# Kernel optimization log

Hardware: AMD Instinct MI355X
Metric: run time of the kernel (lower is better)

Reference implementation:

```python
import jax, jax.numpy as jnp
import numpy as np

NUM_LEVELS = 8
BASE_RES = 16
MAX_RES = 1024
TABLE_SIZE = 2 ** 17
FEAT = 2
ALPHA_SHIFT = 5.0
ALPHA_SCALE = 1.0

_growth = np.exp((np.log(MAX_RES) - np.log(BASE_RES)) / (NUM_LEVELS - 1))
SCALINGS = np.floor(BASE_RES * _growth ** np.arange(NUM_LEVELS)).astype(np.float32)  # per-level grid res
CORNERS = np.array([[(i >> 2) & 1, (i >> 1) & 1, i & 1] for i in range(8)], dtype=np.int32)  # voxel corners
PRIMES = np.array([1, 2654435761, 805459861], dtype=np.uint32)  # nerfstudio hash primes


def hash_encode(pos, table):
    # pos: [N,3] in [0,1]; table: [NUM_LEVELS*TABLE_SIZE, FEAT]
    scaled = pos[:, None, :] * jnp.asarray(SCALINGS)[None, :, None]              # [N,L,3]
    f = jnp.floor(scaled)
    w = scaled - f                                                               # trilinear weights
    idx = f.astype(jnp.int32)[:, :, None, :] + jnp.asarray(CORNERS)[None, None]  # [N,L,8,3]
    h = idx.astype(jnp.uint32) * jnp.asarray(PRIMES)
    hashed = (h[..., 0] ^ h[..., 1] ^ h[..., 2]) % TABLE_SIZE                    # [N,L,8]
    hashed = hashed.astype(jnp.int32) + (jnp.arange(NUM_LEVELS, dtype=jnp.int32) * TABLE_SIZE)[None, :, None]
    feats = table[hashed]                                                        # [N,L,8,F] gather
    cw = jnp.where(jnp.asarray(CORNERS)[None, None] == 1, w[:, :, None, :], 1.0 - w[:, :, None, :]).prod(-1)
    out = (feats * cw[..., None]).sum(2)                                         # [N,L,F]
    return out.reshape(pos.shape[0], NUM_LEVELS * FEAT)


def setup_inputs():
    key = jax.random.key(0)
    ks = jax.random.split(key, 8)
    R, S = 8192, 48
    return {
        "positions": jax.random.normal(ks[0], (R, S, 3), jnp.float32),
        "c2ws": jax.random.normal(ks[1], (R, 3, 4), jnp.float32) * 0.5,
        "aabb": jnp.array([[-1.0, -1.0, -1.0], [1.0, 1.0, 1.0]], jnp.float32),
        "table": jax.random.uniform(ks[2], (NUM_LEVELS * TABLE_SIZE, FEAT), jnp.float32, -1e-4, 1e-4),
        "w1": jax.random.normal(ks[3], (16, 32), jnp.float32) * 0.25,
        "b1": jnp.zeros((32,), jnp.float32),
        "w2": jax.random.normal(ks[4], (32, 16), jnp.float32) * 0.18,
        "b2": jnp.zeros((16,), jnp.float32),
        "hw1": jax.random.normal(ks[5], (16, 64), jnp.float32) * 0.25,
        "hb1": jnp.zeros((64,), jnp.float32),
        "hw2": jax.random.normal(ks[6], (64, 1), jnp.float32) * 0.125,
        "hb2": jnp.zeros((1,), jnp.float32),
    }


def reference(positions, c2ws, aabb, table, w1, b1, w2, b2, hw1, hb1, hw2, hb2):
    R, S = positions.shape[:2]
    rot = c2ws[:, :3, :3]
    trans = c2ws[:, :3, 3]
    rot_t = jnp.swapaxes(rot, 1, 2)                          # w2c rotation = R^T
    t_w2c = -jnp.einsum('rij,rj->ri', rot_t, trans)          # w2c translation = -R^T t
    pos = jnp.einsum('rij,rsj->rsi', rot_t, positions) + t_w2c[:, None, :]
    pos = (pos - aabb[0]) / (aabb[1] - aabb[0])              # SceneBox.get_normalized_positions
    selector = jnp.all((pos > 0.0) & (pos < 1.0), axis=-1)   # inside unit cube
    pos = pos * selector[..., None]
    enc = hash_encode(pos.reshape(-1, 3), table)             # [N, 16]
    h = jax.nn.relu(enc @ w1 + b1) @ w2 + b2                 # mlp_base -> geo features
    o = jax.nn.relu(h @ hw1 + hb1) @ hw2 + hb2               # mlp_head -> alpha logits
    o = o.reshape(R, S, -1)
    return ALPHA_SCALE * jax.nn.sigmoid(o - ALPHA_SHIFT) * selector[..., None]
```

## Files before the change

### kernel.cpp

```cpp
#include <hip/hip_runtime.h>
#include <math.h>
#include <stdint.h>

#define NLEV 8
#define TSIZE 131072
#define TMASK (TSIZE - 1)

__global__ __launch_bounds__(256, 2) void rif_fused(
    const float* __restrict__ positions,
    const float* __restrict__ c2ws,
    const float* __restrict__ aabb,
    const float* __restrict__ table,
    const float* __restrict__ w1, const float* __restrict__ b1,
    const float* __restrict__ w2, const float* __restrict__ b2,
    const float* __restrict__ hw1, const float* __restrict__ hb1,
    const float* __restrict__ hw2, const float* __restrict__ hb2,
    float* __restrict__ out, int total, int S)
{
    __shared__ float sPX[256], sPY[256], sPZ[256];
    __shared__ int   sIdx[256];
    __shared__ int   wbase[4];
    __shared__ int   sCnt;

    int gid = blockIdx.x * 256 + threadIdx.x;
    bool inRange = gid < total;

    float posx = 0.f, posy = 0.f, posz = 0.f;
    bool sel = false;
    if (inRange) {
        int r = gid / S;
        const float* p = positions + (size_t)gid * 3;
        const float* c = c2ws + (size_t)r * 12;
        float px = p[0], py = p[1], pz = p[2];
        float c00 = c[0], c01 = c[1], c02 = c[2],  t0 = c[3];
        float c10 = c[4], c11 = c[5], c12 = c[6],  t1 = c[7];
        float c20 = c[8], c21 = c[9], c22 = c[10], t2 = c[11];

        float m0 = __fadd_rn(__fadd_rn(__fmul_rn(c00, px), __fmul_rn(c10, py)), __fmul_rn(c20, pz));
        float m1 = __fadd_rn(__fadd_rn(__fmul_rn(c01, px), __fmul_rn(c11, py)), __fmul_rn(c21, pz));
        float m2 = __fadd_rn(__fadd_rn(__fmul_rn(c02, px), __fmul_rn(c12, py)), __fmul_rn(c22, pz));
        float n0 = __fadd_rn(__fadd_rn(__fmul_rn(c00, t0), __fmul_rn(c10, t1)), __fmul_rn(c20, t2));
        float n1 = __fadd_rn(__fadd_rn(__fmul_rn(c01, t0), __fmul_rn(c11, t1)), __fmul_rn(c21, t2));
        float n2 = __fadd_rn(__fadd_rn(__fmul_rn(c02, t0), __fmul_rn(c12, t1)), __fmul_rn(c22, t2));
        float x0 = __fsub_rn(m0, n0);
        float x1 = __fsub_rn(m1, n1);
        float x2 = __fsub_rn(m2, n2);

        float a0x = aabb[0], a0y = aabb[1], a0z = aabb[2];
        float a1x = aabb[3], a1y = aabb[4], a1z = aabb[5];
        posx = __fdiv_rn(__fsub_rn(x0, a0x), __fsub_rn(a1x, a0x));
        posy = __fdiv_rn(__fsub_rn(x1, a0y), __fsub_rn(a1y, a0y));
        posz = __fdiv_rn(__fsub_rn(x2, a0z), __fsub_rn(a1z, a0z));
        sel = (posx > 0.f) & (posx < 1.f) & (posy > 0.f) & (posy < 1.f) & (posz > 0.f) & (posz < 1.f);
        if (!sel) out[gid] = 0.f;
    }

    unsigned long long m = __ballot(sel);
    int lane = threadIdx.x & 63;
    int wid  = threadIdx.x >> 6;
    int pre  = __popcll(m & ((1ull << lane) - 1ull));
    if (lane == 0) wbase[wid] = __popcll(m);
    __syncthreads();
    if (threadIdx.x == 0) {
        int s = 0;
        #pragma unroll
        for (int w = 0; w < 4; ++w) { int t = wbase[w]; wbase[w] = s; s += t; }
        sCnt = s;
    }
    __syncthreads();
    if (sel) {
        int slot = wbase[wid] + pre;
        sIdx[slot] = threadIdx.x;
        sPX[slot] = posx; sPY[slot] = posy; sPZ[slot] = posz;
    }
    __syncthreads();

    int cnt = sCnt;
    int t = threadIdx.x;
    if (t >= cnt) return;

    posx = sPX[t]; posy = sPY[t]; posz = sPZ[t];
    int ogid = blockIdx.x * 256 + sIdx[t];

    const float kScale[8] = {16.f, 28.f, 52.f, 95.f, 172.f, 312.f, 565.f, 1024.f};
    float enc[16];

    #pragma unroll
    for (int half = 0; half < 2; ++half) {
        float wxs[4], wys[4], wzs[4];
        float2 ft[4][8];
        #pragma unroll
        for (int l4 = 0; l4 < 4; ++l4) {
            int l = half * 4 + l4;
            float sc = kScale[l];
            float sx = posx * sc, sy = posy * sc, sz = posz * sc;
            float fx = floorf(sx), fy = floorf(sy), fz = floorf(sz);
            wxs[l4] = sx - fx; wys[l4] = sy - fy; wzs[l4] = sz - fz;
            uint32_t ix = (uint32_t)(int)fx, iy = (uint32_t)(int)fy, iz = (uint32_t)(int)fz;
            uint32_t hy0 = iy * 2654435761u, hy1 = hy0 + 2654435761u;
            uint32_t hz0 = iz * 805459861u,  hz1 = hz0 + 805459861u;
            const float2* tab = (const float2*)table + (size_t)l * TSIZE;
            #pragma unroll
            for (int cc = 0; cc < 8; ++cc) {
                uint32_t cx = (cc >> 2) & 1, cy = (cc >> 1) & 1, cz = cc & 1;
                uint32_t hh = ((ix + cx) ^ (cy ? hy1 : hy0) ^ (cz ? hz1 : hz0)) & TMASK;
                ft[l4][cc] = tab[hh];
            }
        }
        __builtin_amdgcn_sched_barrier(0);
        #pragma unroll
        for (int l4 = 0; l4 < 4; ++l4) {
            int l = half * 4 + l4;
            float wx = wxs[l4], wy = wys[l4], wz = wzs[l4];
            float ux = 1.f - wx, uy = 1.f - wy, uz = 1.f - wz;
            float q00 = uy * uz, q01 = uy * wz, q10 = wy * uz, q11 = wy * wz;
            float f0, f1;
            f0 = ft[l4][0].x * (ux * q00); f1 = ft[l4][0].y * (ux * q00);
            f0 = fmaf(ft[l4][1].x, ux * q01, f0); f1 = fmaf(ft[l4][1].y, ux * q01, f1);
            f0 = fmaf(ft[l4][2].x, ux * q10, f0); f1 = fmaf(ft[l4][2].y, ux * q10, f1);
            f0 = fmaf(ft[l4][3].x, ux * q11, f0); f1 = fmaf(ft[l4][3].y, ux * q11, f1);
            f0 = fmaf(ft[l4][4].x, wx * q00, f0); f1 = fmaf(ft[l4][4].y, wx * q00, f1);
            f0 = fmaf(ft[l4][5].x, wx * q01, f0); f1 = fmaf(ft[l4][5].y, wx * q01, f1);
            f0 = fmaf(ft[l4][6].x, wx * q10, f0); f1 = fmaf(ft[l4][6].y, wx * q10, f1);
            f0 = fmaf(ft[l4][7].x, wx * q11, f0); f1 = fmaf(ft[l4][7].y, wx * q11, f1);
            enc[2 * l] = f0;
            enc[2 * l + 1] = f1;
        }
    }

    float h1[32];
    #pragma unroll
    for (int j = 0; j < 32; ++j) h1[j] = b1[j];
    #pragma unroll
    for (int i = 0; i < 16; ++i) {
        float e = enc[i];
        #pragma unroll
        for (int j = 0; j < 32; ++j) h1[j] = fmaf(e, w1[i * 32 + j], h1[j]);
    }
    #pragma unroll
    for (int j = 0; j < 32; ++j) h1[j] = fmaxf(h1[j], 0.f);

    float h2[16];
    #pragma unroll
    for (int j = 0; j < 16; ++j) h2[j] = b2[j];
    #pragma unroll
    for (int i = 0; i < 32; ++i) {
        float e = h1[i];
        #pragma unroll
        for (int j = 0; j < 16; ++j) h2[j] = fmaf(e, w2[i * 16 + j], h2[j]);
    }

    float o = hb2[0];
    #pragma unroll
    for (int j = 0; j < 64; ++j) {
        float acc = hb1[j];
        #pragma unroll
        for (int i = 0; i < 16; ++i) acc = fmaf(h2[i], hw1[i * 64 + j], acc);
        o = fmaf(fmaxf(acc, 0.f), hw2[j], o);
    }

    float x = o - 5.0f;
    out[ogid] = 1.0f / (1.0f + expf(-x));
}

extern "C" void kernel_launch(void* const* d_in, const int* in_sizes, int n_in,
                              void* d_out, int out_size, void* d_ws, size_t ws_size,
                              hipStream_t stream) {
    const float* positions = (const float*)d_in[0];
    const float* c2ws      = (const float*)d_in[1];
    const float* aabb      = (const float*)d_in[2];
    const float* table     = (const float*)d_in[3];
    const float* w1  = (const float*)d_in[4];
    const float* b1  = (const float*)d_in[5];
    const float* w2  = (const float*)d_in[6];
    const float* b2  = (const float*)d_in[7];
    const float* hw1 = (const float*)d_in[8];
    const float* hb1 = (const float*)d_in[9];
    const float* hw2 = (const float*)d_in[10];
    const float* hb2 = (const float*)d_in[11];

    int R = in_sizes[1] / 12;
    int total = in_sizes[0] / 3;
    int S = total / R;

    int threads = 256;
    int blocks = (total + threads - 1) / threads;
    hipLaunchKernelGGL(rif_fused, dim3(blocks), dim3(threads), 0, stream,
                       positions, c2ws, aabb, table,
                       w1, b1, w2, b2, hw1, hb1, hw2, hb2,
                       (float*)d_out, total, S);
}
```

Before: 73.15 us.

## Split hash encoding and MLP into two kernels with per-level thread parallelism

Hash-grid encoding moves to its own kernel, where each of the 8 levels is handled by a separate thread (32 samples × 8 levels per block). Results are written to a workspace buffer as 16 feature planes, which a second kernel reads to run the compacted MLP. The goal is more gather parallelism and lower register pressure in the latency-bound gather phase. The cost is an extra launch, a workspace round trip of 16 floats per sample, and computing the position transform again in every level thread and in the MLP kernel. The fused kernel is kept as a simplified fallback without compaction, used when the workspace is too small.

```diff
diff --git a/kernel.cpp b/kernel.cpp
--- a/kernel.cpp
+++ b/kernel.cpp
@@ -5,6 +5,174 @@
 #define NLEV 8
 #define TSIZE 131072
 #define TMASK (TSIZE - 1)
+
+__device__ __forceinline__ void transform_pos(
+    const float* __restrict__ positions, const float* __restrict__ c2ws,
+    const float* __restrict__ aabb, int gid, int S,
+    float& posx, float& posy, float& posz, bool& sel)
+{
+    int r = gid / S;
+    const float* p = positions + (size_t)gid * 3;
+    const float* c = c2ws + (size_t)r * 12;
+    float px = p[0], py = p[1], pz = p[2];
+    float c00 = c[0], c01 = c[1], c02 = c[2],  t0 = c[3];
+    float c10 = c[4], c11 = c[5], c12 = c[6],  t1 = c[7];
+    float c20 = c[8], c21 = c[9], c22 = c[10], t2 = c[11];
+
+    float m0 = __fadd_rn(__fadd_rn(__fmul_rn(c00, px), __fmul_rn(c10, py)), __fmul_rn(c20, pz));
+    float m1 = __fadd_rn(__fadd_rn(__fmul_rn(c01, px), __fmul_rn(c11, py)), __fmul_rn(c21, pz));
+    float m2 = __fadd_rn(__fadd_rn(__fmul_rn(c02, px), __fmul_rn(c12, py)), __fmul_rn(c22, pz));
+    float n0 = __fadd_rn(__fadd_rn(__fmul_rn(c00, t0), __fmul_rn(c10, t1)), __fmul_rn(c20, t2));
+    float n1 = __fadd_rn(__fadd_rn(__fmul_rn(c01, t0), __fmul_rn(c11, t1)), __fmul_rn(c21, t2));
+    float n2 = __fadd_rn(__fadd_rn(__fmul_rn(c02, t0), __fmul_rn(c12, t1)), __fmul_rn(c22, t2));
+    float x0 = __fsub_rn(m0, n0);
+    float x1 = __fsub_rn(m1, n1);
+    float x2 = __fsub_rn(m2, n2);
+
+    float a0x = aabb[0], a0y = aabb[1], a0z = aabb[2];
+    float a1x = aabb[3], a1y = aabb[4], a1z = aabb[5];
+    posx = __fdiv_rn(__fsub_rn(x0, a0x), __fsub_rn(a1x, a0x));
+    posy = __fdiv_rn(__fsub_rn(x1, a0y), __fsub_rn(a1y, a0y));
+    posz = __fdiv_rn(__fsub_rn(x2, a0z), __fsub_rn(a1z, a0z));
+    sel = (posx > 0.f) & (posx < 1.f) & (posy > 0.f) & (posy < 1.f) & (posz > 0.f) & (posz < 1.f);
+}
+
+__global__ __launch_bounds__(256) void rif_encode(
+    const float* __restrict__ positions,
+    const float* __restrict__ c2ws,
+    const float* __restrict__ aabb,
+    const float* __restrict__ table,
+    float* __restrict__ out,
+    float* __restrict__ encbuf,
+    int total, int S)
+{
+    int s_local = threadIdx.x & 31;
+    int l = threadIdx.x >> 5;
+    int gid = blockIdx.x * 32 + s_local;
+    if (gid >= total) return;
+
+    float posx, posy, posz; bool sel;
+    transform_pos(positions, c2ws, aabb, gid, S, posx, posy, posz, sel);
+    if (!sel) { if (l == 0) out[gid] = 0.f; return; }
+
+    float sc = (l == 0) ? 16.f : (l == 1) ? 28.f : (l == 2) ? 52.f : (l == 3) ? 95.f
+             : (l == 4) ? 172.f : (l == 5) ? 312.f : (l == 6) ? 565.f : 1024.f;
+
+    float sx = posx * sc, sy = posy * sc, sz = posz * sc;
+    float fx = floorf(sx), fy = floorf(sy), fz = floorf(sz);
+    float wx = sx - fx, wy = sy - fy, wz = sz - fz;
+    uint32_t ix = (uint32_t)(int)fx, iy = (uint32_t)(int)fy, iz = (uint32_t)(int)fz;
+    uint32_t hy0 = iy * 2654435761u, hy1 = hy0 + 2654435761u;
+    uint32_t hz0 = iz * 805459861u,  hz1 = hz0 + 805459861u;
+    const float2* tab = (const float2*)table + (size_t)l * TSIZE;
+
+    float2 ft[8];
+    #pragma unroll
+    for (int cc = 0; cc < 8; ++cc) {
+        uint32_t cx = (cc >> 2) & 1, cy = (cc >> 1) & 1, cz = cc & 1;
+        uint32_t hh = ((ix + cx) ^ (cy ? hy1 : hy0) ^ (cz ? hz1 : hz0)) & TMASK;
+        ft[cc] = tab[hh];
+    }
+    __builtin_amdgcn_sched_barrier(0);
+
+    float ux = 1.f - wx, uy = 1.f - wy, uz = 1.f - wz;
+    float q00 = uy * uz, q01 = uy * wz, q10 = wy * uz, q11 = wy * wz;
+    float f0, f1;
+    f0 = ft[0].x * (ux * q00); f1 = ft[0].y * (ux * q00);
+    f0 = fmaf(ft[1].x, ux * q01, f0); f1 = fmaf(ft[1].y, ux * q01, f1);
+    f0 = fmaf(ft[2].x, ux * q10, f0); f1 = fmaf(ft[2].y, ux * q10, f1);
+    f0 = fmaf(ft[3].x, ux * q11, f0); f1 = fmaf(ft[3].y, ux * q11, f1);
+    f0 = fmaf(ft[4].x, wx * q00, f0); f1 = fmaf(ft[4].y, wx * q00, f1);
+    f0 = fmaf(ft[5].x, wx * q01, f0); f1 = fmaf(ft[5].y, wx * q01, f1);
+    f0 = fmaf(ft[6].x, wx * q10, f0); f1 = fmaf(ft[6].y, wx * q10, f1);
+    f0 = fmaf(ft[7].x, wx * q11, f0); f1 = fmaf(ft[7].y, wx * q11, f1);
+
+    encbuf[(size_t)(2 * l) * total + gid] = f0;
+    encbuf[(size_t)(2 * l + 1) * total + gid] = f1;
+}
+
+__global__ __launch_bounds__(256, 2) void rif_mlp(
+    const float* __restrict__ positions,
+    const float* __restrict__ c2ws,
+    const float* __restrict__ aabb,
+    const float* __restrict__ w1, const float* __restrict__ b1,
+    const float* __restrict__ w2, const float* __restrict__ b2,
+    const float* __restrict__ hw1, const float* __restrict__ hb1,
+    const float* __restrict__ hw2, const float* __restrict__ hb2,
+    float* __restrict__ out,
+    const float* __restrict__ encbuf,
+    int total, int S)
+{
+    __shared__ int sIdx[256];
+    __shared__ int wbase[4];
+    __shared__ int sCnt;
+
+    int gid = blockIdx.x * 256 + threadIdx.x;
+    bool sel = false;
+    if (gid < total) {
+        float posx, posy, posz;
+        transform_pos(positions, c2ws, aabb, gid, S, posx, posy, posz, sel);
+    }
+
+    unsigned long long m = __ballot(sel);
+    int lane = threadIdx.x & 63;
+    int wid  = threadIdx.x >> 6;
+    int pre  = __popcll(m & ((1ull << lane) - 1ull));
+    if (lane == 0) wbase[wid] = __popcll(m);
+    __syncthreads();
+    if (threadIdx.x == 0) {
+        int s = 0;
+        #pragma unroll
+        for (int w = 0; w < 4; ++w) { int t = wbase[w]; wbase[w] = s; s += t; }
+        sCnt = s;
+    }
+    __syncthreads();
+    if (sel) sIdx[wbase[wid] + pre] = threadIdx.x;
+    __syncthreads();
+
+    int cnt = sCnt;
+    int t = threadIdx.x;
+    if (t >= cnt) return;
+    int ogid = blockIdx.x * 256 + sIdx[t];
+
+    float enc[16];
+    #pragma unroll
+    for (int j = 0; j < 16; ++j) enc[j] = encbuf[(size_t)j * total + ogid];
+
+    float h1[32];
+    #pragma unroll
+    for (int j = 0; j < 32; ++j) h1[j] = b1[j];
+    #pragma unroll
+    for (int i = 0; i < 16; ++i) {
+        float e = enc[i];
+        #pragma unroll
+        for (int j = 0; j < 32; ++j) h1[j] = fmaf(e, w1[i * 32 + j], h1[j]);
+    }
+    #pragma unroll
+    for (int j = 0; j < 32; ++j) h1[j] = fmaxf(h1[j], 0.f);
+
+    float h2[16];
+    #pragma unroll
+    for (int j = 0; j < 16; ++j) h2[j] = b2[j];
+    #pragma unroll
+    for (int i = 0; i < 32; ++i) {
+        float e = h1[i];
+        #pragma unroll
+        for (int j = 0; j < 16; ++j) h2[j] = fmaf(e, w2[i * 16 + j], h2[j]);
+    }
+
+    float o = hb2[0];
+    #pragma unroll
+    for (int j = 0; j < 64; ++j) {
+        float acc = hb1[j];
+        #pragma unroll
+        for (int i = 0; i < 16; ++i) acc = fmaf(h2[i], hw1[i * 64 + j], acc);
+        o = fmaf(fmaxf(acc, 0.f), hw2[j], o);
+    }
+
+    float x = o - 5.0f;
+    out[ogid] = 1.0f / (1.0f + expf(-x));
+}
 
 __global__ __launch_bounds__(256, 2) void rif_fused(
     const float* __restrict__ positions,
@@ -17,115 +185,36 @@
     const float* __restrict__ hw2, const float* __restrict__ hb2,
     float* __restrict__ out, int total, int S)
 {
-    __shared__ float sPX[256], sPY[256], sPZ[256];
-    __shared__ int   sIdx[256];
-    __shared__ int   wbase[4];
-    __shared__ int   sCnt;
-
     int gid = blockIdx.x * 256 + threadIdx.x;
-    bool inRange = gid < total;
-
-    float posx = 0.f, posy = 0.f, posz = 0.f;
-    bool sel = false;
-    if (inRange) {
-        int r = gid / S;
-        const float* p = positions + (size_t)gid * 3;
-        const float* c = c2ws + (size_t)r * 12;
-        float px = p[0], py = p[1], pz = p[2];
-        float c00 = c[0], c01 = c[1], c02 = c[2],  t0 = c[3];
-        float c10 = c[4], c11 = c[5], c12 = c[6],  t1 = c[7];
-        float c20 = c[8], c21 = c[9], c22 = c[10], t2 = c[11];
-
-        float m0 = __fadd_rn(__fadd_rn(__fmul_rn(c00, px), __fmul_rn(c10, py)), __fmul_rn(c20, pz));
-        float m1 = __fadd_rn(__fadd_rn(__fmul_rn(c01, px), __fmul_rn(c11, py)), __fmul_rn(c21, pz));
-        float m2 = __fadd_rn(__fadd_rn(__fmul_rn(c02, px), __fmul_rn(c12, py)), __fmul_rn(c22, pz));
-        float n0 = __fadd_rn(__fadd_rn(__fmul_rn(c00, t0), __fmul_rn(c10, t1)), __fmul_rn(c20, t2));
-        float n1 = __fadd_rn(__fadd_rn(__fmul_rn(c01, t0), __fmul_rn(c11, t1)), __fmul_rn(c21, t2));
-        float n2 = __fadd_rn(__fadd_rn(__fmul_rn(c02, t0), __fmul_rn(c12, t1)), __fmul_rn(c22, t2));
-        float x0 = __fsub_rn(m0, n0);
-        float x1 = __fsub_rn(m1, n1);
-        float x2 = __fsub_rn(m2, n2);
-
-        float a0x = aabb[0], a0y = aabb[1], a0z = aabb[2];
-        float a1x = aabb[3], a1y = aabb[4], a1z = aabb[5];
-        posx = __fdiv_rn(__fsub_rn(x0, a0x), __fsub_rn(a1x, a0x));
-        posy = __fdiv_rn(__fsub_rn(x1, a0y), __fsub_rn(a1y, a0y));
-        posz = __fdiv_rn(__fsub_rn(x2, a0z), __fsub_rn(a1z, a0z));
-        sel = (posx > 0.f) & (posx < 1.f) & (posy > 0.f) & (posy < 1.f) & (posz > 0.f) & (posz < 1.f);
-        if (!sel) out[gid] = 0.f;
-    }
-
-    unsigned long long m = __ballot(sel);
-    int lane = threadIdx.x & 63;
-    int wid  = threadIdx.x >> 6;
-    int pre  = __popcll(m & ((1ull << lane) - 1ull));
-    if (lane == 0) wbase[wid] = __popcll(m);
-    __syncthreads();
-    if (threadIdx.x == 0) {
-        int s = 0;
-        #pragma unroll
-        for (int w = 0; w < 4; ++w) { int t = wbase[w]; wbase[w] = s; s += t; }
-        sCnt = s;
-    }
-    __syncthreads();
-    if (sel) {
-        int slot = wbase[wid] + pre;
-        sIdx[slot] = threadIdx.x;
-        sPX[slot] = posx; sPY[slot] = posy; sPZ[slot] = posz;
-    }
-    __syncthreads();
-
-    int cnt = sCnt;
-    int t = threadIdx.x;
-    if (t >= cnt) return;
-
-    posx = sPX[t]; posy = sPY[t]; posz = sPZ[t];
-    int ogid = blockIdx.x * 256 + sIdx[t];
+    if (gid >= total) return;
+    float posx, posy, posz; bool sel;
+    transform_pos(positions, c2ws, aabb, gid, S, posx, posy, posz, sel);
+    if (!sel) { out[gid] = 0.f; return; }
 
     const float kScale[8] = {16.f, 28.f, 52.f, 95.f, 172.f, 312.f, 565.f, 1024.f};
     float enc[16];
-
-    #pragma unroll
-    for (int half = 0; half < 2; ++half) {
-        float wxs[4], wys[4], wzs[4];
-        float2 ft[4][8];
-        #pragma unroll
-        for (int l4 = 0; l4 < 4; ++l4) {
-            int l = half * 4 + l4;
-            float sc = kScale[l];
-            float sx = posx * sc, sy = posy * sc, sz = posz * sc;
-            float fx = floorf(sx), fy = floorf(sy), fz = floorf(sz);
-            wxs[l4] = sx - fx; wys[l4] = sy - fy; wzs[l4] = sz - fz;
-            uint32_t ix = (uint32_t)(int)fx, iy = (uint32_t)(int)fy, iz = (uint32_t)(int)fz;
-            uint32_t hy0 = iy * 2654435761u, hy1 = hy0 + 2654435761u;
-            uint32_t hz0 = iz * 805459861u,  hz1 = hz0 + 805459861u;
-            const float2* tab = (const float2*)table + (size_t)l * TSIZE;
-            #pragma unroll
-            for (int cc = 0; cc < 8; ++cc) {
-                uint32_t cx = (cc >> 2) & 1, cy = (cc >> 1) & 1, cz = cc & 1;
-                uint32_t hh = ((ix + cx) ^ (cy ? hy1 : hy0) ^ (cz ? hz1 : hz0)) & TMASK;
-                ft[l4][cc] = tab[hh];
-            }
+    #pragma unroll
+    for (int l = 0; l < NLEV; ++l) {
+        float sc = kScale[l];
+        float sx = posx * sc, sy = posy * sc, sz = posz * sc;
+        float fx = floorf(sx), fy = floorf(sy), fz = floorf(sz);
+        float wx = sx - fx, wy = sy - fy, wz = sz - fz;
+        uint32_t ix = (uint32_t)(int)fx, iy = (uint32_t)(int)fy, iz = (uint32_t)(int)fz;
+        uint32_t hy0 = iy * 2654435761u, hy1 = hy0 + 2654435761u;
+        uint32_t hz0 = iz * 805459861u,  hz1 = hz0 + 805459861u;
+        const float2* tab = (const float2*)table + (size_t)l * TSIZE;
+        float f0 = 0.f, f1 = 0.f;
+        #pragma unroll
+        for (int cc = 0; cc < 8; ++cc) {
+            uint32_t cx = (cc >> 2) & 1, cy = (cc >> 1) & 1, cz = cc & 1;
+            uint32_t hh = ((ix + cx) ^ (cy ? hy1 : hy0) ^ (cz ? hz1 : hz0)) & TMASK;
+            float wgt = (cx ? wx : 1.f - wx) * (cy ? wy : 1.f - wy) * (cz ? wz : 1.f - wz);
+            float2 ftv = tab[hh];
+            f0 = fmaf(ftv.x, wgt, f0);
+            f1 = fmaf(ftv.y, wgt, f1);
         }
-        __builtin_amdgcn_sched_barrier(0);
-        #pragma unroll
-        for (int l4 = 0; l4 < 4; ++l4) {
-            int l = half * 4 + l4;
-            float wx = wxs[l4], wy = wys[l4], wz = wzs[l4];
-            float ux = 1.f - wx, uy = 1.f - wy, uz = 1.f - wz;
-            float q00 = uy * uz, q01 = uy * wz, q10 = wy * uz, q11 = wy * wz;
-            float f0, f1;
-            f0 = ft[l4][0].x * (ux * q00); f1 = ft[l4][0].y * (ux * q00);
-            f0 = fmaf(ft[l4][1].x, ux * q01, f0); f1 = fmaf(ft[l4][1].y, ux * q01, f1);
-            f0 = fmaf(ft[l4][2].x, ux * q10, f0); f1 = fmaf(ft[l4][2].y, ux * q10, f1);
-            f0 = fmaf(ft[l4][3].x, ux * q11, f0); f1 = fmaf(ft[l4][3].y, ux * q11, f1);
-            f0 = fmaf(ft[l4][4].x, wx * q00, f0); f1 = fmaf(ft[l4][4].y, wx * q00, f1);
-            f0 = fmaf(ft[l4][5].x, wx * q01, f0); f1 = fmaf(ft[l4][5].y, wx * q01, f1);
-            f0 = fmaf(ft[l4][6].x, wx * q10, f0); f1 = fmaf(ft[l4][6].y, wx * q10, f1);
-            f0 = fmaf(ft[l4][7].x, wx * q11, f0); f1 = fmaf(ft[l4][7].y, wx * q11, f1);
-            enc[2 * l] = f0;
-            enc[2 * l + 1] = f1;
-        }
+        enc[2 * l] = f0;
+        enc[2 * l + 1] = f1;
     }
 
     float h1[32];
@@ -160,7 +249,7 @@
     }
 
     float x = o - 5.0f;
-    out[ogid] = 1.0f / (1.0f + expf(-x));
+    out[gid] = 1.0f / (1.0f + expf(-x));
 }
 
 extern "C" void kernel_launch(void* const* d_in, const int* in_sizes, int n_in,
@@ -183,10 +272,23 @@
     int total = in_sizes[0] / 3;
     int S = total / R;
 
-    int threads = 256;
-    int blocks = (total + threads - 1) / threads;
-    hipLaunchKernelGGL(rif_fused, dim3(blocks), dim3(threads), 0, stream,
-                       positions, c2ws, aabb, table,
-                       w1, b1, w2, b2, hw1, hb1, hw2, hb2,
-                       (float*)d_out, total, S);
-}
+    size_t needed = (size_t)16 * (size_t)total * sizeof(float);
+    if (ws_size >= needed) {
+        float* encbuf = (float*)d_ws;
+        int blocks1 = (total + 31) / 32;
+        hipLaunchKernelGGL(rif_encode, dim3(blocks1), dim3(256), 0, stream,
+                           positions, c2ws, aabb, table,
+                           (float*)d_out, encbuf, total, S);
+        int blocks2 = (total + 255) / 256;
+        hipLaunchKernelGGL(rif_mlp, dim3(blocks2), dim3(256), 0, stream,
+                           positions, c2ws, aabb,
+                           w1, b1, w2, b2, hw1, hb1, hw2, hb2,
+                           (float*)d_out, encbuf, total, S);
+    } else {
+        int blocks = (total + 255) / 256;
+        hipLaunchKernelGGL(rif_fused, dim3(blocks), dim3(256), 0, stream,
+                           positions, c2ws, aabb, table,
+                           w1, b1, w2, b2, hw1, hb1, hw2, hb2,
+                           (float*)d_out, total, S);
+    }
+}
```

Result: slower. 94.40 us (+29.0%).
